# Performance work log

Hardware: AMD Instinct MI355X
Metric: run time of the kernel (lower is better)

Reference implementation:

```python
import jax, jax.numpy as jnp
import numpy as np

B, N, D, H = 4, 4096, 512, 8
K = D // H  # per-head dim = 64


def setup_inputs() -> dict:
    key = jax.random.key(0)
    k1, k2, k3, k4 = jax.random.split(key, 4)
    x = jax.random.normal(k1, (B, N, D), dtype=jnp.float32)
    # Conv1d(D, K, 1, bias=False) -> weight matrix [K, D], kaiming fan_out
    Wa = jax.random.normal(k2, (K, D), dtype=jnp.float32) * np.float32(np.sqrt(2.0 / K))
    # Conv1d(K, 1, 1) -> weight vector [K], bias scalar (init 0.01)
    Wb = jax.random.normal(k3, (K,), dtype=jnp.float32) * np.float32(np.sqrt(2.0))
    Wc = jax.random.normal(k4, (K,), dtype=jnp.float32) * np.float32(np.sqrt(2.0))
    wb_bias = jnp.full((), 0.01, dtype=jnp.float32)
    wc_bias = jnp.full((), 0.01, dtype=jnp.float32)
    bias = jnp.full((K,), 0.01, dtype=jnp.float32)
    return {"batchinput": x, "Wa": Wa, "Wb": Wb, "wb_bias": wb_bias,
            "Wc": Wc, "wc_bias": wc_bias, "bias": bias}


def reference(batchinput, Wa, Wb, wb_bias, Wc, wc_bias, bias):
    # single step (n_steps=1); all n_head heads share weights, so mean over
    # identical heads equals one head (dropout=0.0 -> identity).
    h = jnp.einsum('bnd,kd->bnk', batchinput, Wa)            # [B,N,K] projected feats
    t1 = jnp.einsum('bnk,k->bn', h, Wb) + wb_bias            # [B,N]
    t2 = jnp.einsum('bnk,k->bn', h, Wc) + wc_bias            # [B,N]
    scores = t1[:, :, None] + t2[:, None, :]                 # [B,N,N] additive score
    coefs = jax.nn.softmax(jax.nn.leaky_relu(scores, negative_slope=0.2), axis=-1)
    out = jnp.einsum('bnm,bmk->bnk', coefs, h) + bias        # [B,N,K]
    return out
```

## Files before the change

kernel.cpp:

```cpp
#include <hip/hip_runtime.h>
#include <hip/hip_bf16.h>

constexpr int cB = 4;
constexpr int cN = 4096;
constexpr int cD = 512;
constexpr int cK = 64;
constexpr int cNB = cB * cN;
constexpr int cNP = cN + 1;
constexpr int cCS = 16;
constexpr int cNC = cN / cCS;
constexpr int cNC1 = cNC + 1;

typedef unsigned short u16;
typedef unsigned int u32;
typedef unsigned long long u64;
typedef __bf16 bf16x8 __attribute__((ext_vector_type(8)));
typedef float f32x4 __attribute__((ext_vector_type(4)));

constexpr size_t OFF_H    = 0;
constexpr size_t OFF_T1   = OFF_H    + (size_t)cNB * cK;
constexpr size_t OFF_T2   = OFF_T1   + cNB;
constexpr size_t OFF_T2S  = OFF_T2   + cNB;
constexpr size_t OFF_IDX  = OFF_T2S  + cNB;
constexpr size_t OFF_EPL  = OFF_IDX  + cNB;
constexpr size_t OFF_GNL  = OFF_EPL  + (size_t)cB * cNP * cK;
constexpr size_t OFF_EPS  = OFF_GNL  + (size_t)cB * cNP * cK;
constexpr size_t OFF_GNS  = OFF_EPS  + (size_t)cB * cNP;
constexpr size_t OFF_CHE  = OFF_GNS  + (size_t)cB * cNP;
constexpr size_t OFF_CHG  = OFF_CHE  + (size_t)cB * cNC * cK;
constexpr size_t OFF_CHES = OFF_CHG  + (size_t)cB * cNC * cK;
constexpr size_t OFF_CHGS = OFF_CHES + (size_t)cB * cNC;
constexpr size_t OFF_OFE  = OFF_CHGS + (size_t)cB * cNC;
constexpr size_t OFF_OFG  = OFF_OFE  + (size_t)cB * cNC1 * cK;
constexpr size_t OFF_OFES = OFF_OFG  + (size_t)cB * cNC1 * cK;
constexpr size_t OFF_OFGS = OFF_OFES + (size_t)cB * cNC1;
constexpr size_t OFF_XB16 = OFF_OFGS + (size_t)cB * cNC1;
constexpr size_t OFF_WB16 = OFF_XB16 + (size_t)cNB * cD / 2;

__device__ __forceinline__ u16 f2bf(float f) {
    unsigned u = __float_as_uint(f);
    u += 0x7fffu + ((u >> 16) & 1u);
    return (u16)(u >> 16);
}
__device__ __forceinline__ u32 pk2(float a, float b) {
    return (u32)f2bf(a) | ((u32)f2bf(b) << 16);
}
__device__ __forceinline__ u32 f2sort(float f) {
    u32 b = __float_as_uint(f);
    u32 mask = (u32)((int)b >> 31);
    return b ^ (mask | 0x80000000u);
}

__global__ __launch_bounds__(256) void k_prep(
    const float* __restrict__ x, const float* __restrict__ Wa,
    const float* __restrict__ Wb, const float* __restrict__ wbb,
    const float* __restrict__ Wc, const float* __restrict__ wcb,
    u16* __restrict__ xb16, u16* __restrict__ wab16,
    float* __restrict__ t1, float* __restrict__ t2)
{
    __shared__ float wabL[cD], wacL[cD];
    int t = threadIdx.x;
    if (blockIdx.x >= 512) {
        int i4 = (((int)blockIdx.x - 512) * 256 + t) * 4;
        float4 v = *(const float4*)(Wa + i4);
        uint2 p = {pk2(v.x, v.y), pk2(v.z, v.w)};
        *(uint2*)(wab16 + i4) = p;
        return;
    }
    float s1a = 0.f, s2a = 0.f, s1b = 0.f, s2b = 0.f;
#pragma unroll 8
    for (int k = 0; k < cK; ++k) {
        float wbk = Wb[k], wck = Wc[k];
        float wa1 = Wa[k * cD + t];
        float wa2 = Wa[k * cD + t + 256];
        s1a += wa1 * wbk; s2a += wa1 * wck;
        s1b += wa2 * wbk; s2b += wa2 * wck;
    }
    wabL[t] = s1a; wacL[t] = s2a; wabL[t + 256] = s1b; wacL[t + 256] = s2b;
    __syncthreads();

    int w = t >> 6, lane = t & 63;
    int d1 = lane * 4, d2 = 256 + lane * 4;
    float4 wbA = *(const float4*)&wabL[d1], wbB = *(const float4*)&wabL[d2];
    float4 wcA = *(const float4*)&wacL[d1], wcB = *(const float4*)&wacL[d2];
    float wbbv = wbb[0], wcbv = wcb[0];
#pragma unroll 2
    for (int rr = 0; rr < 8; ++rr) {
        int row = blockIdx.x * 32 + w * 8 + rr;
        const float* xp = x + (size_t)row * cD;
        float4 a  = *(const float4*)(xp + d1);
        float4 bq = *(const float4*)(xp + d2);
        uint2 pa = {pk2(a.x, a.y), pk2(a.z, a.w)};
        uint2 pb = {pk2(bq.x, bq.y), pk2(bq.z, bq.w)};
        *(uint2*)(xb16 + (size_t)row * cD + d1) = pa;
        *(uint2*)(xb16 + (size_t)row * cD + d2) = pb;
        float p1 = a.x*wbA.x + a.y*wbA.y + a.z*wbA.z + a.w*wbA.w
                 + bq.x*wbB.x + bq.y*wbB.y + bq.z*wbB.z + bq.w*wbB.w;
        float p2 = a.x*wcA.x + a.y*wcA.y + a.z*wcA.z + a.w*wcA.w
                 + bq.x*wcB.x + bq.y*wcB.y + bq.z*wcB.z + bq.w*wcB.w;
#pragma unroll
        for (int off = 32; off > 0; off >>= 1) {
            p1 += __shfl_down(p1, off, 64);
            p2 += __shfl_down(p2, off, 64);
        }
        if (lane == 0) { t1[row] = p1 + wbbv; t2[row] = p2 + wcbv; }
    }
}

__global__ __launch_bounds__(256) void k_projrank(
    const u16* __restrict__ xb16, const u16* __restrict__ wab16,
    const float* __restrict__ t2,
    float* __restrict__ h, float* __restrict__ t2s, int* __restrict__ idxs)
{
    __shared__ u64 shbuf[4096 + 128];
    int t = threadIdx.x;
    if (blockIdx.x < 256) {
        u16* xs = (u16*)shbuf;
        u16* was = xs + 64 * 32;
        int rowbase = blockIdx.x * 64;
        int w = t >> 6, lane = t & 63, m = lane & 15, quad = lane >> 4;
        int grow = w * 16 + (lane >> 2);
        int gcol = (lane & 3) * 8;
        const u16* xg = xb16 + (size_t)(rowbase + grow) * cD + gcol;
        const u16* wg = wab16 + (size_t)grow * cD + gcol;
        int lidx = grow * 32 + gcol;

        f32x4 acc[4] = {{0.f,0.f,0.f,0.f},{0.f,0.f,0.f,0.f},
                        {0.f,0.f,0.f,0.f},{0.f,0.f,0.f,0.f}};
        uint4 xv = *(const uint4*)(xg);
        uint4 wv = *(const uint4*)(wg);
        for (int s = 0; s < 16; ++s) {
            __syncthreads();
            *(uint4*)&xs[lidx] = xv;
            *(uint4*)&was[lidx] = wv;
            if (s < 15) {
                xv = *(const uint4*)(xg + (s + 1) * 32);
                wv = *(const uint4*)(wg + (s + 1) * 32);
            }
            __syncthreads();
            bf16x8 av = *(const bf16x8*)&xs[(w * 16 + m) * 32 + quad * 8];
#pragma unroll
            for (int g = 0; g < 4; ++g) {
                bf16x8 bv = *(const bf16x8*)&was[(g * 16 + m) * 32 + quad * 8];
                acc[g] = __builtin_amdgcn_mfma_f32_16x16x32_bf16(av, bv, acc[g], 0, 0, 0);
            }
        }
#pragma unroll
        for (int g = 0; g < 4; ++g) {
#pragma unroll
            for (int r4 = 0; r4 < 4; ++r4) {
                int row = w * 16 + quad * 4 + r4;
                h[(size_t)(rowbase + row) * cK + g * 16 + m] = acc[g][r4];
            }
        }
    } else {
        u64* keys = shbuf;
        int* part = (int*)(shbuf + 4096);
        int rb = blockIdx.x - 256;
        int b = rb >> 6;
        int rowgrp = rb & 63;
        for (int i = t; i < cN; i += 256)
            keys[i] = ((u64)f2sort(t2[b * cN + i]) << 32) | (u32)i;
        __syncthreads();
        int lane = t & 63, subset = t >> 6;
        u64 mykey = keys[rowgrp * 64 + lane];
        int s0 = subset * 1024;
        int cnt = 0;
#pragma unroll 8
        for (int kk = 0; kk < 1024; ++kk)
            cnt += (keys[s0 + kk] < mykey) ? 1 : 0;
        part[subset * 64 + lane] = cnt;
        __syncthreads();
        if (t < 64) {
            int jj = rowgrp * 64 + t;
            int rank = part[t] + part[64 + t] + part[128 + t] + part[192 + t];
            t2s[b * cN + rank] = t2[b * cN + jj];
            idxs[b * cN + rank] = jj;
        }
    }
}

__global__ __launch_bounds__(64) void k_chunkscan(
    const float* __restrict__ t2s, const int* __restrict__ idxs,
    const float* __restrict__ h,
    float* __restrict__ EpL, float* __restrict__ GnL,
    float* __restrict__ eps_l, float* __restrict__ gns_l,
    float* __restrict__ chE, float* __restrict__ chG,
    float* __restrict__ chEs, float* __restrict__ chGs)
{
    int lane = threadIdx.x;
    int blk = blockIdx.x;
    int c = blk & (cNC - 1);
    int b = blk >> 8;
    int base = b * cN + c * cCS;
    size_t rowbase = ((size_t)b * cNP + c * cCS) * cK;
    int sbase = b * cNP + c * cCS;
    float M2 = t2s[b * cN + cN - 1];
    int   idxv = (lane < cCS) ? idxs[base + lane] : 0;
    float t2v  = (lane < cCS) ? t2s[base + lane] : 0.f;

    float hv[cCS];
#pragma unroll
    for (int i = 0; i < cCS; ++i) {
        int j = __shfl(idxv, i, 64);
        hv[i] = h[((size_t)b * cN + j) * cK + lane];
    }
    float ee[cCS], gg[cCS];
#pragma unroll
    for (int i = 0; i < cCS; ++i) {
        float d = __shfl(t2v, i, 64) - M2;
        ee[i] = __expf(d);
        gg[i] = __expf(0.2f * d);
    }
    if (c == cNC - 1) {
        EpL[((size_t)b * cNP + cN) * cK + lane] = 0.f;
        GnL[((size_t)b * cNP + cN) * cK + lane] = 0.f;
        if (lane == 0) { eps_l[b * cNP + cN] = 0.f; gns_l[b * cNP + cN] = 0.f; }
    }
    float acc = 0.f, accs = 0.f;
#pragma unroll
    for (int i = cCS - 1; i >= 0; --i) {
        acc += ee[i] * hv[i]; accs += ee[i];
        EpL[rowbase + (size_t)i * cK + lane] = acc;
        if (lane == 0) eps_l[sbase + i] = accs;
    }
    chE[((size_t)b * cNC + c) * cK + lane] = acc;
    if (lane == 0) chEs[b * cNC + c] = accs;
    acc = 0.f; accs = 0.f;
#pragma unroll
    for (int i = 0; i < cCS; ++i) {
        GnL[rowbase + (size_t)i * cK + lane] = acc;
        if (lane == 0) gns_l[sbase + i] = accs;
        acc += gg[i] * hv[i]; accs += gg[i];
    }
    chG[((size_t)b * cNC + c) * cK + lane] = acc;
    if (lane == 0) chGs[b * cNC + c] = accs;
}

__global__ __launch_bounds__(256) void k_offsets(
    const float* __restrict__ chE, const float* __restrict__ chG,
    const float* __restrict__ chEs, const float* __restrict__ chGs,
    float* __restrict__ ofE, float* __restrict__ ofG,
    float* __restrict__ ofEs, float* __restrict__ ofGs)
{
    __shared__ float wsum[4][64];
    int t = threadIdx.x;
    int lane = t & 63, w = t >> 6;
    int dir = blockIdx.x & 1;
    int b = blockIdx.x >> 1;
    const float* ch = dir ? chG : chE;
    float* of = dir ? ofG : ofE;
    int c0 = w * 64;

    float cv[64];
    float s = 0.f;
#pragma unroll
    for (int i = 0; i < 64; ++i) {
        cv[i] = ch[((size_t)b * cNC + c0 + i) * cK + lane];
        s += cv[i];
    }
    wsum[w][lane] = s;
    __syncthreads();
    float base = 0.f;
    if (dir == 0) { for (int w2 = w + 1; w2 < 4; ++w2) base += wsum[w2][lane]; }
    else          { for (int w2 = 0; w2 < w; ++w2) base += wsum[w2][lane]; }

    if (dir == 0) {
        float run = base;
#pragma unroll
        for (int i = 63; i >= 0; --i) {
            of[((size_t)b * cNC1 + c0 + i) * cK + lane] = run;
            run += cv[i];
        }
        if (w == 0) of[((size_t)b * cNC1 + cNC) * cK + lane] = 0.f;
    } else {
        float run = base;
#pragma unroll
        for (int i = 0; i < 64; ++i) {
            of[((size_t)b * cNC1 + c0 + i) * cK + lane] = run;
            run += cv[i];
        }
        if (w == 3) of[((size_t)b * cNC1 + cNC) * cK + lane] = run;
    }

    if (w == 0) {
        const float* chs = dir ? chGs : chEs;
        float* ofs = dir ? ofGs : ofEs;
        float e0 = chs[b * cNC + lane * 4 + 0];
        float e1 = chs[b * cNC + lane * 4 + 1];
        float e2 = chs[b * cNC + lane * 4 + 2];
        float e3 = chs[b * cNC + lane * 4 + 3];
        float p = e0 + e1 + e2 + e3;
        if (dir == 0) {
            float s2 = p;
#pragma unroll
            for (int off = 1; off < 64; off <<= 1) {
                float tv = __shfl_down(s2, off, 64);
                if (lane + off < 64) s2 += tv;
            }
            float excl = s2 - p;
            ofs[b * cNC1 + lane * 4 + 0] = excl + e1 + e2 + e3;
            ofs[b * cNC1 + lane * 4 + 1] = excl + e2 + e3;
            ofs[b * cNC1 + lane * 4 + 2] = excl + e3;
            ofs[b * cNC1 + lane * 4 + 3] = excl;
            if (lane == 0) ofs[b * cNC1 + cNC] = 0.f;
        } else {
            float s2 = p;
#pragma unroll
            for (int off = 1; off < 64; off <<= 1) {
                float tv = __shfl_up(s2, off, 64);
                if (lane >= off) s2 += tv;
            }
            float excl = s2 - p;
            ofs[b * cNC1 + lane * 4 + 0] = excl;
            ofs[b * cNC1 + lane * 4 + 1] = excl + e0;
            ofs[b * cNC1 + lane * 4 + 2] = excl + e0 + e1;
            ofs[b * cNC1 + lane * 4 + 3] = excl + e0 + e1 + e2;
            if (lane == 63) ofs[b * cNC1 + cNC] = s2;
        }
    }
}

__global__ __launch_bounds__(256) void k_out(
    const float* __restrict__ t1, const float* __restrict__ t2s,
    const float* __restrict__ EpL, const float* __restrict__ GnL,
    const float* __restrict__ eps_l, const float* __restrict__ gns_l,
    const float* __restrict__ ofE, const float* __restrict__ ofG,
    const float* __restrict__ ofEs, const float* __restrict__ ofGs,
    const float* __restrict__ bias, float* __restrict__ out)
{
    int tid = threadIdx.x;
    int lane = tid & 63;
    int r = blockIdx.x * 4 + (tid >> 6);
    int b = r >> 12;
    float T1 = t1[r];
    float M2 = t2s[b * cN + cN - 1];
    float smax = T1 + M2;
    float m = fmaxf(smax, 0.2f * smax);
    float A  = __expf(smax - m);
    float Cc = __expf(0.2f * smax - m);
    float keyv = -T1;
    int lo = 0, hi = cN;
    while (lo < hi) {
        int mid = (lo + hi) >> 1;
        if (t2s[b * cN + mid] < keyv) lo = mid + 1; else hi = mid;
    }
    int p = lo;
    int c = p >> 4;
    size_t pr = ((size_t)b * cNP + p) * cK + lane;
    size_t cr = ((size_t)b * cNC1 + c) * cK + lane;
    float num = A * (EpL[pr] + ofE[cr]) + Cc * (GnL[pr] + ofG[cr]);
    float den = A * (eps_l[(size_t)b * cNP + p] + ofEs[b * cNC1 + c])
              + Cc * (gns_l[(size_t)b * cNP + p] + ofGs[b * cNC1 + c]);
    out[(size_t)r * cK + lane] = num / den + bias[lane];
}

extern "C" void kernel_launch(void* const* d_in, const int* in_sizes, int n_in,
                              void* d_out, int out_size, void* d_ws, size_t ws_size,
                              hipStream_t stream)
{
    const float* x    = (const float*)d_in[0];
    const float* Wa   = (const float*)d_in[1];
    const float* Wb   = (const float*)d_in[2];
    const float* wbb  = (const float*)d_in[3];
    const float* Wc   = (const float*)d_in[4];
    const float* wcb  = (const float*)d_in[5];
    const float* bias = (const float*)d_in[6];
    float* out = (float*)d_out;

    float* ws = (float*)d_ws;
    float* h     = ws + OFF_H;
    float* t1    = ws + OFF_T1;
    float* t2    = ws + OFF_T2;
    float* t2s   = ws + OFF_T2S;
    int*   idxs  = (int*)(ws + OFF_IDX);
    float* EpL   = ws + OFF_EPL;
    float* GnL   = ws + OFF_GNL;
    float* eps_l = ws + OFF_EPS;
    float* gns_l = ws + OFF_GNS;
    float* chE   = ws + OFF_CHE;
    float* chG   = ws + OFF_CHG;
    float* chEs  = ws + OFF_CHES;
    float* chGs  = ws + OFF_CHGS;
    float* ofE   = ws + OFF_OFE;
    float* ofG   = ws + OFF_OFG;
    float* ofEs  = ws + OFF_OFES;
    float* ofGs  = ws + OFF_OFGS;
    u16*   xb16  = (u16*)(ws + OFF_XB16);
    u16*   wab16 = (u16*)(ws + OFF_WB16);

    k_prep<<<544, 256, 0, stream>>>(x, Wa, Wb, wbb, Wc, wcb, xb16, wab16, t1, t2);
    k_projrank<<<512, 256, 0, stream>>>(xb16, wab16, t2, h, t2s, idxs);
    k_chunkscan<<<cB * cNC, 64, 0, stream>>>(t2s, idxs, h, EpL, GnL, eps_l, gns_l,
                                             chE, chG, chEs, chGs);
    k_offsets<<<cB * 2, 256, 0, stream>>>(chE, chG, chEs, chGs, ofE, ofG, ofEs, ofGs);
    k_out<<<cNB / 4, 256, 0, stream>>>(t1, t2s, EpL, GnL, eps_l, gns_l,
                                       ofE, ofG, ofEs, ofGs, bias, out);
}
```

Baseline: 132.8 us.

## Fuse chunk scan, offsets and output into one persistent kernel with grid barriers

Merges the chunk-scan, offset-scan and output kernels into a single 512-block kernel that uses atomic-counter grid barriers between phases, removing two launch gaps. The per-row binary search over sorted t2 moves into k_projrank as extra rank-counting blocks that compute each row's insertion position by comparison counting. The risk is deadlock or stalls if not all 512 blocks are co-resident, plus the spin-wait cost; the counter is reset in k_prep.

```diff
diff --git a/kernel.cpp b/kernel.cpp
--- a/kernel.cpp
+++ b/kernel.cpp
@@ -36,6 +36,8 @@
 constexpr size_t OFF_OFGS = OFF_OFES + (size_t)cB * cNC1;
 constexpr size_t OFF_XB16 = OFF_OFGS + (size_t)cB * cNC1;
 constexpr size_t OFF_WB16 = OFF_XB16 + (size_t)cNB * cD / 2;
+constexpr size_t OFF_P    = OFF_WB16 + (size_t)cK * cD / 2;
+constexpr size_t OFF_CNT  = OFF_P + cNB;
 
 __device__ __forceinline__ u16 f2bf(float f) {
     unsigned u = __float_as_uint(f);
@@ -49,6 +51,17 @@
     u32 b = __float_as_uint(f);
     u32 mask = (u32)((int)b >> 31);
     return b ^ (mask | 0x80000000u);
+}
+__device__ __forceinline__ void gbar(u32* cnt, u32 target) {
+    __syncthreads();
+    if (threadIdx.x == 0) {
+        __threadfence();
+        atomicAdd(cnt, 1u);
+        while (__hip_atomic_load(cnt, __ATOMIC_ACQUIRE, __HIP_MEMORY_SCOPE_AGENT) < target) {
+            __builtin_amdgcn_s_sleep(2);
+        }
+    }
+    __syncthreads();
 }
 
 __global__ __launch_bounds__(256) void k_prep(
@@ -56,11 +69,12 @@
     const float* __restrict__ Wb, const float* __restrict__ wbb,
     const float* __restrict__ Wc, const float* __restrict__ wcb,
     u16* __restrict__ xb16, u16* __restrict__ wab16,
-    float* __restrict__ t1, float* __restrict__ t2)
+    float* __restrict__ t1, float* __restrict__ t2, u32* __restrict__ cnt)
 {
     __shared__ float wabL[cD], wacL[cD];
     int t = threadIdx.x;
     if (blockIdx.x >= 512) {
+        if (blockIdx.x == 512 && t == 0) cnt[0] = 0;
         int i4 = (((int)blockIdx.x - 512) * 256 + t) * 4;
         float4 v = *(const float4*)(Wa + i4);
         uint2 p = {pk2(v.x, v.y), pk2(v.z, v.w)};
@@ -109,8 +123,9 @@
 
 __global__ __launch_bounds__(256) void k_projrank(
     const u16* __restrict__ xb16, const u16* __restrict__ wab16,
-    const float* __restrict__ t2,
-    float* __restrict__ h, float* __restrict__ t2s, int* __restrict__ idxs)
+    const float* __restrict__ t2, const float* __restrict__ t1,
+    float* __restrict__ h, float* __restrict__ t2s, int* __restrict__ idxs,
+    int* __restrict__ pidx)
 {
     __shared__ u64 shbuf[4096 + 128];
     int t = threadIdx.x;
@@ -153,7 +168,7 @@
                 h[(size_t)(rowbase + row) * cK + g * 16 + m] = acc[g][r4];
             }
         }
-    } else {
+    } else if (blockIdx.x < 512) {
         u64* keys = shbuf;
         int* part = (int*)(shbuf + 4096);
         int rb = blockIdx.x - 256;
@@ -177,182 +192,198 @@
             t2s[b * cN + rank] = t2[b * cN + jj];
             idxs[b * cN + rank] = jj;
         }
-    }
-}
-
-__global__ __launch_bounds__(64) void k_chunkscan(
-    const float* __restrict__ t2s, const int* __restrict__ idxs,
-    const float* __restrict__ h,
+    } else {
+        float* keysf = (float*)shbuf;
+        int* part = (int*)(shbuf + 2048);
+        int rb = blockIdx.x - 512;
+        int b = rb >> 6;
+        int rowgrp = rb & 63;
+        for (int i = t; i < cN; i += 256)
+            keysf[i] = t2[b * cN + i];
+        __syncthreads();
+        int lane = t & 63, subset = t >> 6;
+        float key = -t1[b * cN + rowgrp * 64 + lane];
+        int s0 = subset * 1024;
+        int cnt = 0;
+#pragma unroll 8
+        for (int kk = 0; kk < 1024; ++kk)
+            cnt += (keysf[s0 + kk] < key) ? 1 : 0;
+        part[subset * 64 + lane] = cnt;
+        __syncthreads();
+        if (t < 64) {
+            pidx[b * cN + rowgrp * 64 + t] =
+                part[t] + part[64 + t] + part[128 + t] + part[192 + t];
+        }
+    }
+}
+
+__global__ __launch_bounds__(256, 2) void k_backend(
+    const float* __restrict__ t1, const float* __restrict__ t2s,
+    const int* __restrict__ idxs, const float* __restrict__ h,
+    const int* __restrict__ pidx,
     float* __restrict__ EpL, float* __restrict__ GnL,
     float* __restrict__ eps_l, float* __restrict__ gns_l,
     float* __restrict__ chE, float* __restrict__ chG,
-    float* __restrict__ chEs, float* __restrict__ chGs)
-{
-    int lane = threadIdx.x;
-    int blk = blockIdx.x;
-    int c = blk & (cNC - 1);
-    int b = blk >> 8;
-    int base = b * cN + c * cCS;
-    size_t rowbase = ((size_t)b * cNP + c * cCS) * cK;
-    int sbase = b * cNP + c * cCS;
-    float M2 = t2s[b * cN + cN - 1];
-    int   idxv = (lane < cCS) ? idxs[base + lane] : 0;
-    float t2v  = (lane < cCS) ? t2s[base + lane] : 0.f;
-
-    float hv[cCS];
-#pragma unroll
-    for (int i = 0; i < cCS; ++i) {
-        int j = __shfl(idxv, i, 64);
-        hv[i] = h[((size_t)b * cN + j) * cK + lane];
-    }
-    float ee[cCS], gg[cCS];
-#pragma unroll
-    for (int i = 0; i < cCS; ++i) {
-        float d = __shfl(t2v, i, 64) - M2;
-        ee[i] = __expf(d);
-        gg[i] = __expf(0.2f * d);
-    }
-    if (c == cNC - 1) {
-        EpL[((size_t)b * cNP + cN) * cK + lane] = 0.f;
-        GnL[((size_t)b * cNP + cN) * cK + lane] = 0.f;
-        if (lane == 0) { eps_l[b * cNP + cN] = 0.f; gns_l[b * cNP + cN] = 0.f; }
-    }
-    float acc = 0.f, accs = 0.f;
-#pragma unroll
-    for (int i = cCS - 1; i >= 0; --i) {
-        acc += ee[i] * hv[i]; accs += ee[i];
-        EpL[rowbase + (size_t)i * cK + lane] = acc;
-        if (lane == 0) eps_l[sbase + i] = accs;
-    }
-    chE[((size_t)b * cNC + c) * cK + lane] = acc;
-    if (lane == 0) chEs[b * cNC + c] = accs;
-    acc = 0.f; accs = 0.f;
-#pragma unroll
-    for (int i = 0; i < cCS; ++i) {
-        GnL[rowbase + (size_t)i * cK + lane] = acc;
-        if (lane == 0) gns_l[sbase + i] = accs;
-        acc += gg[i] * hv[i]; accs += gg[i];
-    }
-    chG[((size_t)b * cNC + c) * cK + lane] = acc;
-    if (lane == 0) chGs[b * cNC + c] = accs;
-}
-
-__global__ __launch_bounds__(256) void k_offsets(
-    const float* __restrict__ chE, const float* __restrict__ chG,
-    const float* __restrict__ chEs, const float* __restrict__ chGs,
+    float* __restrict__ chEs, float* __restrict__ chGs,
     float* __restrict__ ofE, float* __restrict__ ofG,
-    float* __restrict__ ofEs, float* __restrict__ ofGs)
+    float* __restrict__ ofEs, float* __restrict__ ofGs,
+    const float* __restrict__ bias, float* __restrict__ out,
+    u32* __restrict__ cnt)
 {
     __shared__ float wsum[4][64];
     int t = threadIdx.x;
     int lane = t & 63, w = t >> 6;
-    int dir = blockIdx.x & 1;
-    int b = blockIdx.x >> 1;
-    const float* ch = dir ? chG : chE;
-    float* of = dir ? ofG : ofE;
-    int c0 = w * 64;
-
-    float cv[64];
-    float s = 0.f;
-#pragma unroll
-    for (int i = 0; i < 64; ++i) {
-        cv[i] = ch[((size_t)b * cNC + c0 + i) * cK + lane];
-        s += cv[i];
-    }
-    wsum[w][lane] = s;
-    __syncthreads();
-    float base = 0.f;
-    if (dir == 0) { for (int w2 = w + 1; w2 < 4; ++w2) base += wsum[w2][lane]; }
-    else          { for (int w2 = 0; w2 < w; ++w2) base += wsum[w2][lane]; }
-
-    if (dir == 0) {
-        float run = base;
-#pragma unroll
-        for (int i = 63; i >= 0; --i) {
-            of[((size_t)b * cNC1 + c0 + i) * cK + lane] = run;
-            run += cv[i];
-        }
-        if (w == 0) of[((size_t)b * cNC1 + cNC) * cK + lane] = 0.f;
-    } else {
-        float run = base;
+
+    {
+        int gw = blockIdx.x * 4 + w;
+        int dir = gw >> 10;
+        int b = (gw >> 8) & 3;
+        int c = gw & 255;
+        int base = b * cN + c * cCS;
+        size_t rowbase = ((size_t)b * cNP + c * cCS) * cK;
+        int sbase = b * cNP + c * cCS;
+        float M2 = t2s[b * cN + cN - 1];
+        int   idxv = (lane < cCS) ? idxs[base + lane] : 0;
+        float t2v  = (lane < cCS) ? t2s[base + lane] : 0.f;
+        float hv[cCS];
+#pragma unroll
+        for (int i = 0; i < cCS; ++i) {
+            int j = __shfl(idxv, i, 64);
+            hv[i] = h[((size_t)b * cN + j) * cK + lane];
+        }
+        if (dir == 0) {
+            float ee[cCS];
+#pragma unroll
+            for (int i = 0; i < cCS; ++i)
+                ee[i] = __expf(__shfl(t2v, i, 64) - M2);
+            if (c == cNC - 1) {
+                EpL[((size_t)b * cNP + cN) * cK + lane] = 0.f;
+                if (lane == 0) eps_l[b * cNP + cN] = 0.f;
+            }
+            float acc = 0.f, accs = 0.f;
+#pragma unroll
+            for (int i = cCS - 1; i >= 0; --i) {
+                acc += ee[i] * hv[i]; accs += ee[i];
+                EpL[rowbase + (size_t)i * cK + lane] = acc;
+                if (lane == 0) eps_l[sbase + i] = accs;
+            }
+            chE[((size_t)b * cNC + c) * cK + lane] = acc;
+            if (lane == 0) chEs[b * cNC + c] = accs;
+        } else {
+            float gg[cCS];
+#pragma unroll
+            for (int i = 0; i < cCS; ++i)
+                gg[i] = __expf(0.2f * (__shfl(t2v, i, 64) - M2));
+            if (c == cNC - 1) {
+                GnL[((size_t)b * cNP + cN) * cK + lane] = 0.f;
+                if (lane == 0) gns_l[b * cNP + cN] = 0.f;
+            }
+            float acc = 0.f, accs = 0.f;
+#pragma unroll
+            for (int i = 0; i < cCS; ++i) {
+                GnL[rowbase + (size_t)i * cK + lane] = acc;
+                if (lane == 0) gns_l[sbase + i] = accs;
+                acc += gg[i] * hv[i]; accs += gg[i];
+            }
+            chG[((size_t)b * cNC + c) * cK + lane] = acc;
+            if (lane == 0) chGs[b * cNC + c] = accs;
+        }
+    }
+    gbar(cnt, 512);
+
+    if (blockIdx.x < 8) {
+        int dir = blockIdx.x & 1;
+        int b = blockIdx.x >> 1;
+        const float* ch = dir ? chG : chE;
+        float* of = dir ? ofG : ofE;
+        int c0 = w * 64;
+        float cv[64];
+        float s = 0.f;
 #pragma unroll
         for (int i = 0; i < 64; ++i) {
-            of[((size_t)b * cNC1 + c0 + i) * cK + lane] = run;
-            run += cv[i];
-        }
-        if (w == 3) of[((size_t)b * cNC1 + cNC) * cK + lane] = run;
-    }
-
-    if (w == 0) {
-        const float* chs = dir ? chGs : chEs;
-        float* ofs = dir ? ofGs : ofEs;
-        float e0 = chs[b * cNC + lane * 4 + 0];
-        float e1 = chs[b * cNC + lane * 4 + 1];
-        float e2 = chs[b * cNC + lane * 4 + 2];
-        float e3 = chs[b * cNC + lane * 4 + 3];
-        float p = e0 + e1 + e2 + e3;
+            cv[i] = ch[((size_t)b * cNC + c0 + i) * cK + lane];
+            s += cv[i];
+        }
+        wsum[w][lane] = s;
+        __syncthreads();
+        float base = 0.f;
+        if (dir == 0) { for (int w2 = w + 1; w2 < 4; ++w2) base += wsum[w2][lane]; }
+        else          { for (int w2 = 0; w2 < w; ++w2) base += wsum[w2][lane]; }
         if (dir == 0) {
-            float s2 = p;
-#pragma unroll
-            for (int off = 1; off < 64; off <<= 1) {
-                float tv = __shfl_down(s2, off, 64);
-                if (lane + off < 64) s2 += tv;
-            }
-            float excl = s2 - p;
-            ofs[b * cNC1 + lane * 4 + 0] = excl + e1 + e2 + e3;
-            ofs[b * cNC1 + lane * 4 + 1] = excl + e2 + e3;
-            ofs[b * cNC1 + lane * 4 + 2] = excl + e3;
-            ofs[b * cNC1 + lane * 4 + 3] = excl;
-            if (lane == 0) ofs[b * cNC1 + cNC] = 0.f;
+            float run = base;
+#pragma unroll
+            for (int i = 63; i >= 0; --i) {
+                of[((size_t)b * cNC1 + c0 + i) * cK + lane] = run;
+                run += cv[i];
+            }
+            if (w == 0) of[((size_t)b * cNC1 + cNC) * cK + lane] = 0.f;
         } else {
-            float s2 = p;
-#pragma unroll
-            for (int off = 1; off < 64; off <<= 1) {
-                float tv = __shfl_up(s2, off, 64);
-                if (lane >= off) s2 += tv;
-            }
-            float excl = s2 - p;
-            ofs[b * cNC1 + lane * 4 + 0] = excl;
-            ofs[b * cNC1 + lane * 4 + 1] = excl + e0;
-            ofs[b * cNC1 + lane * 4 + 2] = excl + e0 + e1;
-            ofs[b * cNC1 + lane * 4 + 3] = excl + e0 + e1 + e2;
-            if (lane == 63) ofs[b * cNC1 + cNC] = s2;
-        }
-    }
-}
-
-__global__ __launch_bounds__(256) void k_out(
-    const float* __restrict__ t1, const float* __restrict__ t2s,
-    const float* __restrict__ EpL, const float* __restrict__ GnL,
-    const float* __restrict__ eps_l, const float* __restrict__ gns_l,
-    const float* __restrict__ ofE, const float* __restrict__ ofG,
-    const float* __restrict__ ofEs, const float* __restrict__ ofGs,
-    const float* __restrict__ bias, float* __restrict__ out)
-{
-    int tid = threadIdx.x;
-    int lane = tid & 63;
-    int r = blockIdx.x * 4 + (tid >> 6);
-    int b = r >> 12;
-    float T1 = t1[r];
-    float M2 = t2s[b * cN + cN - 1];
-    float smax = T1 + M2;
-    float m = fmaxf(smax, 0.2f * smax);
-    float A  = __expf(smax - m);
-    float Cc = __expf(0.2f * smax - m);
-    float keyv = -T1;
-    int lo = 0, hi = cN;
-    while (lo < hi) {
-        int mid = (lo + hi) >> 1;
-        if (t2s[b * cN + mid] < keyv) lo = mid + 1; else hi = mid;
-    }
-    int p = lo;
-    int c = p >> 4;
-    size_t pr = ((size_t)b * cNP + p) * cK + lane;
-    size_t cr = ((size_t)b * cNC1 + c) * cK + lane;
-    float num = A * (EpL[pr] + ofE[cr]) + Cc * (GnL[pr] + ofG[cr]);
-    float den = A * (eps_l[(size_t)b * cNP + p] + ofEs[b * cNC1 + c])
-              + Cc * (gns_l[(size_t)b * cNP + p] + ofGs[b * cNC1 + c]);
-    out[(size_t)r * cK + lane] = num / den + bias[lane];
+            float run = base;
+#pragma unroll
+            for (int i = 0; i < 64; ++i) {
+                of[((size_t)b * cNC1 + c0 + i) * cK + lane] = run;
+                run += cv[i];
+            }
+            if (w == 3) of[((size_t)b * cNC1 + cNC) * cK + lane] = run;
+        }
+        if (w == 0) {
+            const float* chs = dir ? chGs : chEs;
+            float* ofs = dir ? ofGs : ofEs;
+            float e0 = chs[b * cNC + lane * 4 + 0];
+            float e1 = chs[b * cNC + lane * 4 + 1];
+            float e2 = chs[b * cNC + lane * 4 + 2];
+            float e3 = chs[b * cNC + lane * 4 + 3];
+            float p = e0 + e1 + e2 + e3;
+            if (dir == 0) {
+                float s2 = p;
+#pragma unroll
+                for (int off = 1; off < 64; off <<= 1) {
+                    float tv = __shfl_down(s2, off, 64);
+                    if (lane + off < 64) s2 += tv;
+                }
+                float excl = s2 - p;
+                ofs[b * cNC1 + lane * 4 + 0] = excl + e1 + e2 + e3;
+                ofs[b * cNC1 + lane * 4 + 1] = excl + e2 + e3;
+                ofs[b * cNC1 + lane * 4 + 2] = excl + e3;
+                ofs[b * cNC1 + lane * 4 + 3] = excl;
+                if (lane == 0) ofs[b * cNC1 + cNC] = 0.f;
+            } else {
+                float s2 = p;
+#pragma unroll
+                for (int off = 1; off < 64; off <<= 1) {
+                    float tv = __shfl_up(s2, off, 64);
+                    if (lane >= off) s2 += tv;
+                }
+                float excl = s2 - p;
+                ofs[b * cNC1 + lane * 4 + 0] = excl;
+                ofs[b * cNC1 + lane * 4 + 1] = excl + e0;
+                ofs[b * cNC1 + lane * 4 + 2] = excl + e0 + e1;
+                ofs[b * cNC1 + lane * 4 + 3] = excl + e0 + e1 + e2;
+                if (lane == 63) ofs[b * cNC1 + cNC] = s2;
+            }
+        }
+    }
+    gbar(cnt, 1024);
+
+#pragma unroll 2
+    for (int g = 0; g < 8; ++g) {
+        int r = g * 2048 + blockIdx.x * 4 + w;
+        int b = r >> 12;
+        float T1 = t1[r];
+        float M2 = t2s[b * cN + cN - 1];
+        float smax = T1 + M2;
+        float m = fmaxf(smax, 0.2f * smax);
+        float A  = __expf(smax - m);
+        float Cc = __expf(0.2f * smax - m);
+        int p = pidx[r];
+        int c = p >> 4;
+        size_t pr = ((size_t)b * cNP + p) * cK + lane;
+        size_t cr = ((size_t)b * cNC1 + c) * cK + lane;
+        float num = A * (EpL[pr] + ofE[cr]) + Cc * (GnL[pr] + ofG[cr]);
+        float den = A * (eps_l[(size_t)b * cNP + p] + ofEs[b * cNC1 + c])
+                  + Cc * (gns_l[(size_t)b * cNP + p] + ofGs[b * cNC1 + c]);
+        out[(size_t)r * cK + lane] = num / den + bias[lane];
+    }
 }
 
 extern "C" void kernel_launch(void* const* d_in, const int* in_sizes, int n_in,
@@ -388,12 +419,14 @@
     float* ofGs  = ws + OFF_OFGS;
     u16*   xb16  = (u16*)(ws + OFF_XB16);
     u16*   wab16 = (u16*)(ws + OFF_WB16);
-
-    k_prep<<<544, 256, 0, stream>>>(x, Wa, Wb, wbb, Wc, wcb, xb16, wab16, t1, t2);
-    k_projrank<<<512, 256, 0, stream>>>(xb16, wab16, t2, h, t2s, idxs);
-    k_chunkscan<<<cB * cNC, 64, 0, stream>>>(t2s, idxs, h, EpL, GnL, eps_l, gns_l,
-                                             chE, chG, chEs, chGs);
-    k_offsets<<<cB * 2, 256, 0, stream>>>(chE, chG, chEs, chGs, ofE, ofG, ofEs, ofGs);
-    k_out<<<cNB / 4, 256, 0, stream>>>(t1, t2s, EpL, GnL, eps_l, gns_l,
-                                       ofE, ofG, ofEs, ofGs, bias, out);
-}
+    int*   pidx  = (int*)(ws + OFF_P);
+    u32*   cnt   = (u32*)(ws + OFF_CNT);
+
+    k_prep<<<544, 256, 0, stream>>>(x, Wa, Wb, wbb, Wc, wcb, xb16, wab16, t1, t2, cnt);
+    k_projrank<<<768, 256, 0, stream>>>(xb16, wab16, t2, t1, h, t2s, idxs, pidx);
+    k_backend<<<512, 256, 0, stream>>>(t1, t2s, idxs, h, pidx,
+                                       EpL, GnL, eps_l, gns_l,
+                                       chE, chG, chEs, chGs,
+                                       ofE, ofG, ofEs, ofGs,
+                                       bias, out, cnt);
+}
```

Result: slower. 218.7 us (+64.7%).
